# Performance work log

Measured on AMD Instinct MI355X. Metric: run time of the kernel, lower is better.

Reference implementation:

```python
import jax, jax.numpy as jnp
import numpy as np

D = 256          # object_dim == query_dim
HG = 1024        # g hidden / output width
HF0, HF1 = 1024, 512
OUT_F = 256
N = 32768        # number of objects


def _mlp_g(h, W0, b0, W1, b1, W2, b2):
    # g=True: ReLU after every layer, including output.
    h = jax.nn.relu(h @ W0 + b0)
    h = jax.nn.relu(h @ W1 + b1)
    return jax.nn.relu(h @ W2 + b2)


def _mlp_f(h, W0, b0, W1, b1, W2, b2):
    # f: ReLU on hidden layers, linear output.
    h = jax.nn.relu(h @ W0 + b0)
    h = jax.nn.relu(h @ W1 + b1)
    return h @ W2 + b2


def setup_inputs() -> dict:
    key = jax.random.key(0)
    ks = jax.random.split(key, 16)
    def lin(k, fan_in, fan_out):
        s = 1.0 / np.sqrt(fan_in)
        kw, kb = jax.random.split(k)
        W = jax.random.uniform(kw, (fan_in, fan_out), jnp.float32, -s, s)
        b = jax.random.uniform(kb, (fan_out,), jnp.float32, -s, s)
        return W, b
    x = jax.random.normal(ks[0], (N, D), jnp.float32)
    q = jax.random.normal(ks[1], (D,), jnp.float32)
    g_W0, g_b0 = lin(ks[2], 3 * D, HG)
    g_W1, g_b1 = lin(ks[3], HG, HG)
    g_W2, g_b2 = lin(ks[4], HG, HG)
    f_W0, f_b0 = lin(ks[5], HG, HF0)
    f_W1, f_b1 = lin(ks[6], HF0, HF1)
    f_W2, f_b2 = lin(ks[7], HF1, OUT_F)
    return dict(x=x, q=q,
                g_W0=g_W0, g_b0=g_b0, g_W1=g_W1, g_b1=g_b1, g_W2=g_W2, g_b2=g_b2,
                f_W0=f_W0, f_b0=f_b0, f_W1=f_W1, f_b1=f_b1, f_W2=f_W2, f_b2=f_b2)


def reference(x, q, g_W0, g_b0, g_W1, g_b1, g_W2, g_b2,
              f_W0, f_b0, f_W1, f_b1, f_W2, f_b2):
    n = x.shape[0]
    # mode 4: adjacent pairs (o_i, o_{i+1}), query concatenated to each pair.
    pair_concat = jnp.concatenate(
        [x[:-1], x[1:], jnp.broadcast_to(q, (n - 1, q.shape[0]))], axis=-1)  # (n-1, 3D)
    relations = _mlp_g(pair_concat, g_W0, g_b0, g_W1, g_b1, g_W2, g_b2)       # (n-1, HG)
    embedding = jnp.sum(relations, axis=0)                                     # (HG,)
    return _mlp_f(embedding, f_W0, f_b0, f_W1, f_b1, f_W2, f_b2)               # (OUT_F,)
```

## Files before the change

kernel.cpp:

```cpp
#include <hip/hip_runtime.h>

typedef __attribute__((ext_vector_type(8))) short short8;
typedef __attribute__((ext_vector_type(4))) float floatx4;
typedef __attribute__((ext_vector_type(4))) unsigned int uint32x4;

#define NROWS 32768L
#define NVALID 32767L
#define HGDIM 1024

__device__ __forceinline__ unsigned short f2bf_rne(float f) {
    union { float f; unsigned u; } v; v.f = f;
    unsigned r = v.u + 0x7fffu + ((v.u >> 16) & 1u);
    return (unsigned short)(r >> 16);
}

__device__ __forceinline__ void gload_lds16(const void* g, void* l) {
    __builtin_amdgcn_global_load_lds(
        (const __attribute__((address_space(1))) void*)g,
        (__attribute__((address_space(3))) void*)l,
        16, 0, 0);
}

__global__ void cvt_x(const float* __restrict__ x, unsigned short* __restrict__ xb,
                      long nx, long ntot4) {
    long i = (long)blockIdx.x * 256 + threadIdx.x;
    if (i >= ntot4) return;
    long i4 = i * 4;
    float4 v = make_float4(0.f, 0.f, 0.f, 0.f);
    if (i4 < nx) v = *(const float4*)(x + i4);
    ushort4 o;
    o.x = f2bf_rne(v.x); o.y = f2bf_rne(v.y); o.z = f2bf_rne(v.z); o.w = f2bf_rne(v.w);
    *(ushort4*)(xb + i4) = o;
}

__global__ void transpose_cvt(const float* __restrict__ W, unsigned short* __restrict__ Wt,
                              int K, int N) {
    __shared__ float tile[32][33];
    int tx = threadIdx.x & 31, ty = threadIdx.x >> 5;
    int nb = blockIdx.x * 32, kb = blockIdx.y * 32;
    #pragma unroll
    for (int i = 0; i < 32; i += 8)
        tile[ty + i][tx] = W[(size_t)(kb + ty + i) * N + (nb + tx)];
    __syncthreads();
    #pragma unroll
    for (int i = 0; i < 32; i += 8)
        Wt[(size_t)(nb + ty + i) * K + (kb + tx)] = f2bf_rne(tile[tx][ty + i]);
}

template<bool RELU_IN>
__global__ void fc_partial(const float* __restrict__ in, const float* __restrict__ W,
                           const float* __restrict__ bias, float* __restrict__ out,
                           int N) {
    __shared__ float s_in[128];
    int j = blockIdx.x * 256 + threadIdx.x;
    int k0 = blockIdx.y * 128;
    if (threadIdx.x < 128) {
        float v = in[k0 + threadIdx.x];
        if (RELU_IN) v = fmaxf(v, 0.f);
        s_in[threadIdx.x] = v;
    }
    __syncthreads();
    float acc = (blockIdx.y == 0) ? bias[j] : 0.f;
    #pragma unroll 4
    for (int k = 0; k < 128; ++k)
        acc += s_in[k] * W[(size_t)(k0 + k) * N + j];
    atomicAdd(&out[j], acc);
}


#define SBAR() __builtin_amdgcn_sched_barrier(0)

#define P_PRE(N) do { SBAR(); __builtin_amdgcn_s_barrier(); \
    asm volatile("s_waitcnt lgkmcnt(" #N ")" ::: "memory"); SBAR(); \
    __builtin_amdgcn_s_setprio(1); } while (0)

#define P_POST() do { __builtin_amdgcn_s_setprio(0); SBAR(); \
    __builtin_amdgcn_s_barrier(); SBAR(); } while (0)

#define P_POSTV0() do { __builtin_amdgcn_s_setprio(0); SBAR(); \
    asm volatile("s_waitcnt vmcnt(0)" ::: "memory"); SBAR(); \
    __builtin_amdgcn_s_barrier(); SBAR(); } while (0)

#define STAGE(buf, region, T) do { \
    if ((region) >= 2) { \
        const unsigned short* _g = gA + (long)(((region) & 1) * 128) * lda + (long)(T) * 64; \
        char* _d = (char*)&lds[buf][0][((region) & 1) * 128][0] + t * 16; \
        gload_lds16(_g, _d); \
        gload_lds16(_g + 64L * lda, _d + 8192); \
    } else { \
        const unsigned short* _g = gB + (long)(((region) & 1) * 128) * ldb + (long)(T) * 64; \
        char* _d = (char*)&lds[buf][1][((region) & 1) * 128][0] + t * 16; \
        gload_lds16(_g, _d); \
        gload_lds16(_g + 64L * ldb, _d + 8192); \
    } } while (0)

#define LDA4(dst, buf, mbase, ks) do { _Pragma("unroll") for (int _q = 0; _q < 4; ++_q) \
    dst[_q] = *(const short8*)((const char*)&lds[buf][0][arowb + ((mbase) + _q) * 16][0] + ((ks) ? cb1 : cb0)); } while (0)

#define LDB4(dst, buf, ks) do { _Pragma("unroll") for (int _q = 0; _q < 4; ++_q) \
    dst[_q] = *(const short8*)((const char*)&lds[buf][1][browb + _q * 16][0] + ((ks) ? cb1 : cb0)); } while (0)

#define MFMA16(AF, BF, MO) do { _Pragma("unroll") for (int _mf = 0; _mf < 4; ++_mf) { \
    _Pragma("unroll") for (int _nf = 0; _nf < 4; ++_nf) \
        acc[(MO) + _mf][_nf] = __builtin_amdgcn_mfma_f32_16x16x32_bf16(AF[_mf], BF[_nf], acc[(MO) + _mf][_nf], 0, 0, 0); } } while (0)

template<int COLSUM>
__global__ __launch_bounds__(512, 2)
void gemm256(const unsigned short* __restrict__ A, int lda,
             const unsigned short* __restrict__ Bt, int ldb,
             const float* __restrict__ bias, int K,
             unsigned short* __restrict__ Hout,
             float* __restrict__ emb, long row0g, long nvalid,
             int mblocks) {
    __shared__ alignas(16) unsigned short lds[2][2][256][64];

    const int t = threadIdx.x;
    int nwg = gridDim.x, bid = blockIdx.x, swz;
    if ((nwg & 7) == 0) { int cpx = nwg >> 3; swz = (bid & 7) * cpx + (bid >> 3); }
    else swz = bid;
    const int mb = swz >> 2, nb = swz & 3;
    const long m0 = (long)mb * 256;
    const int n0 = nb * 256;

    const int srow = t >> 3;
    const int ssc = (t & 7) ^ (srow & 7);
    const unsigned short* gA = A + (m0 + srow) * (long)lda + ssc * 8;
    const unsigned short* gB = Bt + ((long)n0 + srow) * (long)ldb + ssc * 8;

    const int lane = t & 63;
    const int wv = t >> 6;
    const int wm = wv >> 2, wn = wv & 3;
    const int arowb = wm * 128 + (lane & 15);
    const int browb = wn * 64 + (lane & 15);
    const int c0x = (lane >> 4) ^ (lane & 7);
    const int cb0 = c0x * 16;
    const int cb1 = (c0x ^ 4) * 16;

    floatx4 acc[8][4] = {};

    const int NT = K >> 6;
    const int NI = NT >> 1;

    short8 bE0[4], bE1[4], bO0[4], bO1[4];
    short8 aE0[4], aE1[4], aE2[4], aE3[4], aO0[4], aO1[4], aO2[4], aO3[4];

    STAGE(0, 0, 0); STAGE(0, 1, 0); STAGE(0, 2, 0); STAGE(0, 3, 0);
    STAGE(1, 0, 1); STAGE(1, 1, 1);
    asm volatile("s_waitcnt vmcnt(4)" ::: "memory");
    SBAR();
    __builtin_amdgcn_s_barrier();
    SBAR();
    LDB4(bE0, 0, 0); LDA4(aE0, 0, 0, 0);

    for (int i = 0; i < NI; ++i) {
        const int O = 2 * i + 1;
        int N2 = 2 * i + 2; if (N2 >= NT) N2 = 0;
        int P2 = 2 * i + 3; if (P2 >= NT) P2 = 1;

        STAGE(1, 2, O); STAGE(1, 3, O);
        LDA4(aE1, 0, 4, 0);
        P_PRE(4); MFMA16(aE0, bE0, 0); P_POST();
        LDB4(bE1, 0, 1); LDA4(aE2, 0, 0, 1);
        P_PRE(8); MFMA16(aE1, bE0, 4); P_POST();
        LDA4(aE3, 0, 4, 1);
        P_PRE(4); MFMA16(aE2, bE1, 0); P_POSTV0();
        STAGE(0, 0, N2); STAGE(0, 1, N2);
        LDB4(bO0, 1, 0); LDA4(aO0, 1, 0, 0);
        P_PRE(8); MFMA16(aE3, bE1, 4); P_POST();
        STAGE(0, 2, N2); STAGE(0, 3, N2);
        LDA4(aO1, 1, 4, 0);
        P_PRE(4); MFMA16(aO0, bO0, 0); P_POST();
        LDB4(bO1, 1, 1); LDA4(aO2, 1, 0, 1);
        P_PRE(8); MFMA16(aO1, bO0, 4); P_POST();
        LDA4(aO3, 1, 4, 1);
        P_PRE(4); MFMA16(aO2, bO1, 0); P_POSTV0();
        STAGE(1, 0, P2); STAGE(1, 1, P2);
        LDB4(bE0, 0, 0); LDA4(aE0, 0, 0, 0);
        P_PRE(8); MFMA16(aO3, bO1, 4); P_POST();
    }
    asm volatile("s_waitcnt vmcnt(0) lgkmcnt(0)" ::: "memory");
    SBAR();
    __builtin_amdgcn_s_barrier();

    if (COLSUM == 0) {
        char* slb = (char*)&lds[0][0][0][0];
        #pragma unroll
        for (int nf = 0; nf < 4; ++nf) {
            int ncol = wn * 64 + nf * 16 + (lane & 15);
            float bv = bias[n0 + ncol];
            #pragma unroll
            for (int mf = 0; mf < 8; ++mf) {
                int rbase = wm * 128 + mf * 16 + ((lane >> 4) << 2);
                #pragma unroll
                for (int j = 0; j < 4; ++j) {
                    int row = rbase + j;
                    float v = fmaxf(acc[mf][nf][j] + bv, 0.f);
                    int byte = row * 512 + ((ncol * 2) ^ ((row & 7) << 4));
                    *(unsigned short*)(slb + byte) = f2bf_rne(v);
                }
            }
        }
        __syncthreads();
        {
            int rsub = t >> 5;
            int cb = (t & 31) * 16;
            #pragma unroll
            for (int i2 = 0; i2 < 16; ++i2) {
                int row = i2 * 16 + rsub;
                const char* src = slb + row * 512 + (cb ^ ((row & 7) << 4));
                uint32x4 v = *(const uint32x4*)src;
                char* dst = (char*)Hout + ((size_t)(m0 + row) * HGDIM + n0) * 2 + cb;
                *(uint32x4*)dst = v;
            }
        }
    } else {
        #pragma unroll
        for (int nf = 0; nf < 4; ++nf) {
            int ncol = n0 + wn * 64 + nf * 16 + (lane & 15);
            float bv = bias[ncol];
            float cs = 0.f;
            #pragma unroll
            for (int mf = 0; mf < 8; ++mf) {
                long rbase = row0g + m0 + wm * 128 + mf * 16 + ((lane >> 4) << 2);
                #pragma unroll
                for (int j = 0; j < 4; ++j) {
                    float v = fmaxf(acc[mf][nf][j] + bv, 0.f);
                    if (rbase + j < nvalid) cs += v;
                }
            }
            cs += __shfl_xor(cs, 16);
            cs += __shfl_xor(cs, 32);
            if ((lane >> 4) == 0) atomicAdd(&emb[ncol], cs);
        }
    }
}

extern "C" void kernel_launch(void* const* d_in, const int* in_sizes, int n_in,
                              void* d_out, int out_size, void* d_ws, size_t ws_size,
                              hipStream_t stream) {
    const float* x   = (const float*)d_in[0];
    const float* q   = (const float*)d_in[1];
    const float* gW0 = (const float*)d_in[2];
    const float* gb0 = (const float*)d_in[3];
    const float* gW1 = (const float*)d_in[4];
    const float* gb1 = (const float*)d_in[5];
    const float* gW2 = (const float*)d_in[6];
    const float* gb2 = (const float*)d_in[7];
    const float* fW0 = (const float*)d_in[8];
    const float* fb0 = (const float*)d_in[9];
    const float* fW1 = (const float*)d_in[10];
    const float* fb1 = (const float*)d_in[11];
    const float* fW2 = (const float*)d_in[12];
    const float* fb2 = (const float*)d_in[13];
    float* out = (float*)d_out;

    char* ws = (char*)d_ws;
    size_t off = 0;
    auto alloc = [&](size_t bytes) -> char* {
        char* p = ws + off;
        off += (bytes + 255) & ~(size_t)255;
        return p;
    };
    unsigned short* xb  = (unsigned short*)alloc((NROWS + 1) * 256 * 2);
    unsigned short* w0t = (unsigned short*)alloc((size_t)1024 * 512 * 2);
    unsigned short* w1t = (unsigned short*)alloc((size_t)1024 * 1024 * 2);
    unsigned short* w2t = (unsigned short*)alloc((size_t)1024 * 1024 * 2);
    float* c0  = (float*)alloc(4096);
    float* emb = (float*)alloc(4096);
    float* e1  = (float*)alloc(4096);
    float* e2  = (float*)alloc(4096);
    size_t fixed = off;
    size_t avail = (ws_size > fixed) ? ws_size - fixed : 0;
    long CR = (long)((avail / 2) / (HGDIM * 2));
    CR = (CR / 512) * 512;
    if (CR > NROWS) CR = NROWS;
    if (CR < 512) CR = 512;
    unsigned short* H0 = (unsigned short*)alloc((size_t)CR * HGDIM * 2);
    unsigned short* H1 = (unsigned short*)alloc((size_t)CR * HGDIM * 2);

    hipMemsetAsync(c0, 0, 4 * 4096, stream);
    hipMemsetAsync(out, 0, 256 * sizeof(float), stream);

    long ntot4 = (NROWS + 1) * 256 / 4;
    cvt_x<<<dim3((unsigned)((ntot4 + 255) / 256)), 256, 0, stream>>>(x, xb, NROWS * 256, ntot4);

    transpose_cvt<<<dim3(32, 16), 256, 0, stream>>>(gW0, w0t, 512, 1024);
    transpose_cvt<<<dim3(32, 32), 256, 0, stream>>>(gW1, w1t, 1024, 1024);
    transpose_cvt<<<dim3(32, 32), 256, 0, stream>>>(gW2, w2t, 1024, 1024);

    fc_partial<false><<<dim3(4, 2), 256, 0, stream>>>(q, gW0 + (size_t)512 * 1024, gb0, c0, 1024);

    for (long r0 = 0; r0 < NROWS; r0 += CR) {
        long rows = NROWS - r0; if (rows > CR) rows = CR;
        int mblocks = (int)(rows / 256);
        dim3 g((unsigned)(mblocks * 4));
        gemm256<0><<<g, 512, 0, stream>>>(xb + r0 * 256, 256, w0t, 512, c0, 512,
                                          H0, nullptr, 0, 0, mblocks);
        gemm256<0><<<g, 512, 0, stream>>>(H0, 1024, w1t, 1024, gb1, 1024,
                                          H1, nullptr, 0, 0, mblocks);
        gemm256<1><<<g, 512, 0, stream>>>(H1, 1024, w2t, 1024, gb2, 1024,
                                          nullptr, emb, r0, NVALID, mblocks);
    }

    fc_partial<false><<<dim3(4, 8), 256, 0, stream>>>(emb, fW0, fb0, e1, 1024);
    fc_partial<true><<<dim3(2, 8), 256, 0, stream>>>(e1, fW1, fb1, e2, 512);
    fc_partial<true><<<dim3(1, 4), 256, 0, stream>>>(e2, fW2, fb2, out, 256);
}
```

Measured before the change: 245.9 us.

## Interleave global-to-LDS stage loads one per MFMA phase with partial vmcnt waits

Spreads the eight STAGE global-to-LDS loads per iteration evenly, one before each MFMA phase, instead of issuing them in pairs. The two full vmcnt(0) drains are replaced with partial vmcnt(4) or vmcnt(2) waits at every phase barrier. The aim is to smooth memory traffic and hide load latency behind matrix work without stalling for all outstanding loads. It relies on the wait counts exactly matching the new issue order, and any miscount could let an LDS region be read before it is fully written.

```diff
diff --git a/kernel.cpp b/kernel.cpp
--- a/kernel.cpp
+++ b/kernel.cpp
@@ -74,11 +74,8 @@
     asm volatile("s_waitcnt lgkmcnt(" #N ")" ::: "memory"); SBAR(); \
     __builtin_amdgcn_s_setprio(1); } while (0)
 
-#define P_POST() do { __builtin_amdgcn_s_setprio(0); SBAR(); \
-    __builtin_amdgcn_s_barrier(); SBAR(); } while (0)
-
-#define P_POSTV0() do { __builtin_amdgcn_s_setprio(0); SBAR(); \
-    asm volatile("s_waitcnt vmcnt(0)" ::: "memory"); SBAR(); \
+#define P_POSTW(N) do { __builtin_amdgcn_s_setprio(0); SBAR(); \
+    asm volatile("s_waitcnt vmcnt(" #N ")" ::: "memory"); SBAR(); \
     __builtin_amdgcn_s_barrier(); SBAR(); } while (0)
 
 #define STAGE(buf, region, T) do { \
@@ -157,26 +154,30 @@
         int N2 = 2 * i + 2; if (N2 >= NT) N2 = 0;
         int P2 = 2 * i + 3; if (P2 >= NT) P2 = 1;
 
-        STAGE(1, 2, O); STAGE(1, 3, O);
         LDA4(aE1, 0, 4, 0);
-        P_PRE(4); MFMA16(aE0, bE0, 0); P_POST();
+        STAGE(1, 2, O);
+        P_PRE(4); MFMA16(aE0, bE0, 0); P_POSTW(4);
         LDB4(bE1, 0, 1); LDA4(aE2, 0, 0, 1);
-        P_PRE(8); MFMA16(aE1, bE0, 4); P_POST();
+        STAGE(1, 3, O);
+        P_PRE(8); MFMA16(aE1, bE0, 4); P_POSTW(4);
         LDA4(aE3, 0, 4, 1);
-        P_PRE(4); MFMA16(aE2, bE1, 0); P_POSTV0();
-        STAGE(0, 0, N2); STAGE(0, 1, N2);
+        STAGE(0, 0, N2);
+        P_PRE(4); MFMA16(aE2, bE1, 0); P_POSTW(4);
         LDB4(bO0, 1, 0); LDA4(aO0, 1, 0, 0);
-        P_PRE(8); MFMA16(aE3, bE1, 4); P_POST();
-        STAGE(0, 2, N2); STAGE(0, 3, N2);
+        STAGE(0, 1, N2);
+        P_PRE(8); MFMA16(aE3, bE1, 4); P_POSTW(4);
         LDA4(aO1, 1, 4, 0);
-        P_PRE(4); MFMA16(aO0, bO0, 0); P_POST();
+        STAGE(0, 2, N2);
+        P_PRE(4); MFMA16(aO0, bO0, 0); P_POSTW(4);
         LDB4(bO1, 1, 1); LDA4(aO2, 1, 0, 1);
-        P_PRE(8); MFMA16(aO1, bO0, 4); P_POST();
+        STAGE(0, 3, N2);
+        P_PRE(8); MFMA16(aO1, bO0, 4); P_POSTW(4);
         LDA4(aO3, 1, 4, 1);
-        P_PRE(4); MFMA16(aO2, bO1, 0); P_POSTV0();
-        STAGE(1, 0, P2); STAGE(1, 1, P2);
+        STAGE(1, 0, P2);
+        P_PRE(4); MFMA16(aO2, bO1, 0); P_POSTW(2);
         LDB4(bE0, 0, 0); LDA4(aE0, 0, 0, 0);
-        P_PRE(8); MFMA16(aO3, bO1, 4); P_POST();
+        STAGE(1, 1, P2);
+        P_PRE(8); MFMA16(aO3, bO1, 4); P_POSTW(4);
     }
     asm volatile("s_waitcnt vmcnt(0) lgkmcnt(0)" ::: "memory");
     SBAR();
```

After: 241.1 us. About the same (-2.0%).
